# Kernel tuning notes

Hardware: AMD Instinct MI355X
Metric: run time of the kernel (lower is better)

## Reference

```python
import jax, jax.numpy as jnp
import numpy as np
from jax import lax

NUM_CLASSES = 102
IN_CAPS = 2592
IN_DIM = 8
OUT_DIM = 16
ROUTINGS = 3
IMG = 112

def squash(s, axis=-1, eps=1e-8):
    sq = jnp.sum(s * s, axis=axis, keepdims=True)
    return (sq / (1.0 + sq)) * s / jnp.sqrt(sq + eps)

def conv2d(x, w, b, stride):
    y = lax.conv_general_dilated(x, w, (stride, stride), 'VALID',
                                 dimension_numbers=('NCHW', 'OIHW', 'NCHW'))
    return y + b[None, :, None, None]

def setup_inputs() -> dict:
    key = jax.random.key(0)
    ks = jax.random.split(key, 12)
    B = 32
    x = jax.random.normal(ks[0], (B, 3, IMG, IMG), jnp.float32)
    targets = jax.random.randint(ks[1], (B,), 0, NUM_CLASSES)
    conv1_w = jax.random.normal(ks[2], (256, 3, 11, 11), jnp.float32) * 0.02
    conv1_b = jnp.zeros((256,), jnp.float32)
    pc_w = jax.random.normal(ks[3], (256, 256, 9, 9), jnp.float32) * 0.02
    pc_b = jnp.zeros((256,), jnp.float32)
    W = jax.random.normal(ks[4], (NUM_CLASSES, IN_CAPS, OUT_DIM, IN_DIM), jnp.float32) * 0.01
    fc1_w = jax.random.normal(ks[5], (NUM_CLASSES * OUT_DIM, 512), jnp.float32) * 0.02
    fc1_b = jnp.zeros((512,), jnp.float32)
    fc2_w = jax.random.normal(ks[6], (512, 1024), jnp.float32) * 0.02
    fc2_b = jnp.zeros((1024,), jnp.float32)
    fc3_w = jax.random.normal(ks[7], (1024, 3 * IMG * IMG), jnp.float32) * 0.02
    fc3_b = jnp.zeros((3 * IMG * IMG,), jnp.float32)
    return dict(x=x, targets=targets, conv1_w=conv1_w, conv1_b=conv1_b,
                pc_w=pc_w, pc_b=pc_b, W=W,
                fc1_w=fc1_w, fc1_b=fc1_b, fc2_w=fc2_w, fc2_b=fc2_b,
                fc3_w=fc3_w, fc3_b=fc3_b)

def reference(x, targets, conv1_w, conv1_b, pc_w, pc_b, W,
              fc1_w, fc1_b, fc2_w, fc2_b, fc3_w, fc3_b):
    B = x.shape[0]
    # conv backbone: [B,3,112,112] -> [B,256,34,34]
    feat = jax.nn.relu(conv2d(x, conv1_w, conv1_b, 3))
    # primary caps conv: -> [B,256,9,9] -> [B,2592,8], squash
    pc = conv2d(feat, pc_w, pc_b, 3)
    u = squash(pc.reshape(B, IN_CAPS, IN_DIM))
    # prediction vectors: [B, O, N, D_out]
    x_hat = jnp.einsum('ondi,bni->bond', W, u)
    x_hat_sg = lax.stop_gradient(x_hat)
    b = jnp.zeros((B, NUM_CLASSES, IN_CAPS), x.dtype)
    v = None
    for it in range(ROUTINGS):
        c = jax.nn.softmax(b, axis=1)  # couple over out caps
        xh = x_hat if it == ROUTINGS - 1 else x_hat_sg
        s = jnp.einsum('bon,bond->bod', c, xh)
        v = squash(s)
        if it < ROUTINGS - 1:
            b = b + jnp.einsum('bond,bod->bon', xh, v)
    # reconstruction: mask by target class capsule
    mask = jax.nn.one_hot(targets, NUM_CLASSES, dtype=v.dtype)
    h = (v * mask[:, :, None]).reshape(B, NUM_CLASSES * OUT_DIM)
    h = jax.nn.relu(h @ fc1_w + fc1_b)
    h = jax.nn.relu(h @ fc2_w + fc2_b)
    recon = jax.nn.sigmoid(h @ fc3_w + fc3_b).reshape(B, 3, IMG, IMG)
    return (v, recon)
```

## Files before the change

kernel.cpp:

```cpp
#include <hip/hip_runtime.h>
#include <hip/hip_fp16.h>
#include <math.h>

#define B32   32
#define OCLS  102
#define NCAPS 2592

#define OFF_FEAT   0u
#define OFF_C1WT   10027008u
#define OFF_PCWQ   10076160u
#define OFF_PCP    11780096u
#define OFF_WQ2    17088512u
#define OFF_WQ     25555456u
#define OFF_U2     34022400u
#define OFF_CT     34685952u
#define OFF_DEN    38916096u
#define OFF_S      38999040u
#define OFF_V0     39051264u
#define OFF_V1     39103488u
#define OFF_VSQ    39155712u
#define OFF_H1     39168768u
#define OFF_H2T    39185152u
#define OFF_FC3P   39217920u

typedef __attribute__((ext_vector_type(8))) short short8;
typedef __attribute__((ext_vector_type(4))) float f32x4;
typedef long long i64;

__device__ __forceinline__ unsigned short f2b(float f) {
  union { float f; unsigned u; } v; v.f = f;
  unsigned r = v.u + 0x7fffu + ((v.u >> 16) & 1u);
  return (unsigned short)(r >> 16);
}

__device__ __forceinline__ unsigned f2q_fast(float x) {
  union { float f; unsigned u; } v; v.f = x;
  unsigned s = (v.u >> 24) & 0x80u;
  unsigned au = v.u & 0x7fffffffu;
  if (au < 0x3c800000u) return s;
  if (au >= 0x43e00000u) return s | 0x7eu;
  unsigned r = au + 0x7ffffu + ((au >> 20) & 1u);
  unsigned e = (r >> 23) - 120u;
  unsigned m = (r >> 20) & 7u;
  return s | (e << 3) | m;
}

__device__ __forceinline__ unsigned fp8pair(float a, float b) {
#if __has_builtin(__builtin_amdgcn_cvt_pk_fp8_f32)
  return (unsigned)__builtin_amdgcn_cvt_pk_fp8_f32(a, b, 0, false) & 0xffffu;
#else
  return f2q_fast(a) | (f2q_fast(b) << 8);
#endif
}

__device__ __forceinline__ float rcpf(float x) {
#if __has_builtin(__builtin_amdgcn_rcpf)
  return __builtin_amdgcn_rcpf(x);
#else
  return 1.0f / x;
#endif
}

__global__ __launch_bounds__(256) void k_pack(const float* __restrict__ conv1_w,
                                              const float* __restrict__ pc_w,
                                              const float* __restrict__ W,
                                              unsigned short* __restrict__ C1WB,
                                              unsigned char* __restrict__ PCWQ,
                                              unsigned char* __restrict__ Wq2,
                                              unsigned char* __restrict__ Wq) {
  __shared__ unsigned char sq[32 * 128];
  int bb = blockIdx.x;
  int t = threadIdx.x;
  if (bb < 256) {
    if (t < 128) {
#pragma unroll
      for (int ci = 0; ci < 3; ++ci) {
        float v = (t < 121) ? conv1_w[bb * 363 + ci * 121 + t] : 0.f;
        C1WB[(ci * 256 + bb) * 128 + t] = f2b(v);
      }
    }
  } else if (bb < 512) {
    int co = bb - 256;
    for (int e = t; e < 20736; e += 256) {
      int ci = e / 81, tap = e - ci * 81;
      PCWQ[(size_t)ci * 26624 + co * 104 + tap] =
          (unsigned char)f2q_fast(pc_w[(size_t)co * 20736 + e] * 64.f);
    }
    for (int tap = 81; tap < 104; ++tap)
      PCWQ[(size_t)t * 26624 + co * 104 + tap] = 0;
  } else {
    size_t base = (size_t)(bb - 512) * 4096;
    const float4* src = (const float4*)(W + base + (size_t)t * 16);
    float4 f0 = src[0], f1 = src[1], f2 = src[2], f3 = src[3];
    float v[16] = {f0.x, f0.y, f0.z, f0.w, f1.x, f1.y, f1.z, f1.w,
                   f2.x, f2.y, f2.z, f2.w, f3.x, f3.y, f3.z, f3.w};
    unsigned words[4];
#pragma unroll
    for (int j = 0; j < 4; ++j)
      words[j] = fp8pair(v[4 * j] * 64.f, v[4 * j + 1] * 64.f) |
                 (fp8pair(v[4 * j + 2] * 64.f, v[4 * j + 3] * 64.f) << 16);
    *(uint4*)(Wq2 + base + (size_t)t * 16) =
        make_uint4(words[0], words[1], words[2], words[3]);
    int r = t >> 3, seg = t & 7;
#pragma unroll
    for (int e = 0; e < 16; ++e) {
      unsigned byte = (words[e >> 2] >> ((e & 3) * 8)) & 0xffu;
      int idx = seg * 16 + e, d = idx >> 3, i = idx & 7;
      sq[r * 128 + i * 16 + d] = (unsigned char)byte;
    }
    __syncthreads();
    *(uint4*)(Wq + base + (size_t)t * 16) = ((const uint4*)sq)[t];
  }
}

__global__ __launch_bounds__(256) void k_c1m(const float* __restrict__ x,
                                             const unsigned short* __restrict__ C1WB,
                                             const float* __restrict__ bias,
                                             float* __restrict__ feat2) {
  __shared__ unsigned short sh[48 * 128 + 128 * 128];
  unsigned short* lA = sh;
  unsigned short* lB = sh + 48 * 128;
  float* obuf = (float*)(sh + 48 * 128);

  int bx = blockIdx.x;
  int hf = blockIdx.y;
  int b = bx / 34, ho = bx % 34;
  int t = threadIdx.x;
  int lane = t & 63, wv = t >> 6;
  int l15 = lane & 15, lh = lane >> 4;
  int rx = l15 & 7;

  {
    uint4 zz = make_uint4(0, 0, 0, 0);
    uint4* z = (uint4*)lA;
    for (int i = t; i < 48 * 128 / 8; i += 256) z[i] = zz;
  }
  __syncthreads();

  f32x4 acc[3][2];
#pragma unroll
  for (int mf = 0; mf < 3; ++mf)
#pragma unroll
    for (int nf = 0; nf < 2; ++nf) acc[mf][nf] = (f32x4){0.f, 0.f, 0.f, 0.f};

#pragma unroll 1
  for (int ci = 0; ci < 3; ++ci) {
    {
      const uint4* Bsrc = (const uint4*)(C1WB + ci * 32768 + hf * 16384);
#pragma unroll
      for (int i = 0; i < 8; ++i) {
        int f = i * 256 + t;
        int row = f >> 4, cu = f & 15;
        ((uint4*)lB)[row * 16 + (cu ^ (row & 7))] = Bsrc[f];
      }
    }
    for (int tk = t; tk < 374; tk += 256) {
      int kh = tk / 34, wo = tk - kh * 34;
      const float* src = x + ((size_t)(b * 3 + ci) * 112 + ho * 3 + kh) * 112 + wo * 3;
#pragma unroll
      for (int j = 0; j < 11; ++j) {
        int tap = kh * 11 + j;
        int cu = tap >> 3;
        lA[wo * 128 + (((cu ^ (wo & 7)) << 3) | (tap & 7))] = f2b(src[j]);
      }
    }
    __syncthreads();

#pragma unroll
    for (int s = 0; s < 4; ++s) {
      int cub = ((s * 4 + lh) ^ rx) << 3;
      short8 a0 = *(const short8*)(lA + (0 + l15) * 128 + cub);
      short8 a1 = *(const short8*)(lA + (16 + l15) * 128 + cub);
      short8 a2 = *(const short8*)(lA + (32 + l15) * 128 + cub);
      short8 b0 = *(const short8*)(lB + (wv * 32 + 0 + l15) * 128 + cub);
      short8 b1 = *(const short8*)(lB + (wv * 32 + 16 + l15) * 128 + cub);
      acc[0][0] = __builtin_amdgcn_mfma_f32_16x16x32_bf16(a0, b0, acc[0][0], 0, 0, 0);
      acc[0][1] = __builtin_amdgcn_mfma_f32_16x16x32_bf16(a0, b1, acc[0][1], 0, 0, 0);
      acc[1][0] = __builtin_amdgcn_mfma_f32_16x16x32_bf16(a1, b0, acc[1][0], 0, 0, 0);
      acc[1][1] = __builtin_amdgcn_mfma_f32_16x16x32_bf16(a1, b1, acc[1][1], 0, 0, 0);
      acc[2][0] = __builtin_amdgcn_mfma_f32_16x16x32_bf16(a2, b0, acc[2][0], 0, 0, 0);
      acc[2][1] = __builtin_amdgcn_mfma_f32_16x16x32_bf16(a2, b1, acc[2][1], 0, 0, 0);
    }
    __syncthreads();
  }

  float bv[2];
#pragma unroll
  for (int nf = 0; nf < 2; ++nf) bv[nf] = bias[hf * 128 + wv * 32 + nf * 16 + l15];
#pragma unroll
  for (int mf = 0; mf < 3; ++mf)
#pragma unroll
    for (int nf = 0; nf < 2; ++nf)
#pragma unroll
      for (int r = 0; r < 4; ++r) {
        int wo = mf * 16 + lh * 4 + r;
        if (wo < 36)
          obuf[(wv * 32 + nf * 16 + l15) * 36 + wo] = fmaxf(acc[mf][nf][r] + bv[nf], 0.f);
      }
  __syncthreads();
  float4* dst = (float4*)(feat2 + (size_t)bx * 9216 + hf * 4608);
  const float4* srcb = (const float4*)obuf;
  for (int i = t; i < 1152; i += 256) dst[i] = srcb[i];
}

__device__ __forceinline__ void pc_gather8(const float* __restrict__ feat2,
                                           unsigned char* __restrict__ dstbuf,
                                           int mb, int ci, int t) {
  for (int task = t; task < 576; task += 256) {
    int m = task / 9, kh = task - m * 9;
    int gm = mb * 64 + m;
    if (gm < 2592) {
      int b = gm / 81, p = gm - b * 81;
      int ho = p / 9, wo = p - ho * 9;
      const float* src = feat2 + ((size_t)(b * 34 + ho * 3 + kh) * 256 + ci) * 36 + wo * 3;
      unsigned char* dst = dstbuf + m * 104 + kh * 9;
      unsigned p01 = fp8pair(src[0], src[1]);
      unsigned p23 = fp8pair(src[2], src[3]);
      unsigned p45 = fp8pair(src[4], src[5]);
      unsigned p67 = fp8pair(src[6], src[7]);
      unsigned p8  = fp8pair(src[8], 0.f);
      dst[0] = p01; dst[1] = p01 >> 8;
      dst[2] = p23; dst[3] = p23 >> 8;
      dst[4] = p45; dst[5] = p45 >> 8;
      dst[6] = p67; dst[7] = p67 >> 8;
      dst[8] = p8;
    }
  }
}

__global__ __launch_bounds__(256, 3) void k_pc4(const float* __restrict__ feat2,
                                                const unsigned char* __restrict__ PCWQ,
                                                __half* __restrict__ pcp) {
  __shared__ unsigned char lA[2][64 * 104];

  int mb = blockIdx.x, kc = blockIdx.y;
  int t = threadIdx.x;
  int lane = t & 63, wv = t >> 6;
  int l15 = lane & 15, lh = lane >> 4;

  {
    uint4 zz = make_uint4(0, 0, 0, 0);
    uint4* z = (uint4*)lA;
    for (int i = t; i < 2 * 64 * 104 / 16; i += 256) z[i] = zz;
  }
  __syncthreads();
  pc_gather8(feat2, lA[0], mb, kc * 16, t);
  __syncthreads();

  f32x4 acc[4][4];
#pragma unroll
  for (int mf = 0; mf < 4; ++mf)
#pragma unroll
    for (int nf = 0; nf < 4; ++nf) acc[mf][nf] = (f32x4){0.f, 0.f, 0.f, 0.f};

#pragma unroll 1
  for (int cil = 0; cil < 16; ++cil) {
    int ci = kc * 16 + cil;
    int cur = cil & 1;

    i64 bfr[4][3];
    const unsigned char* Bbase = PCWQ + (size_t)ci * 26624 + (wv * 64 + l15) * 104 + lh * 8;
#pragma unroll
    for (int nf = 0; nf < 4; ++nf)
#pragma unroll
      for (int s = 0; s < 3; ++s)
        bfr[nf][s] = *(const i64*)(Bbase + nf * 16 * 104 + s * 32);

    if (cil < 15) pc_gather8(feat2, lA[cur ^ 1], mb, ci + 1, t);

    const unsigned char* arow = lA[cur] + l15 * 104 + lh * 8;
#pragma unroll
    for (int s = 0; s < 3; ++s) {
      i64 a0 = *(const i64*)(arow + s * 32);
      i64 a1 = *(const i64*)(arow + 16 * 104 + s * 32);
      i64 a2 = *(const i64*)(arow + 32 * 104 + s * 32);
      i64 a3 = *(const i64*)(arow + 48 * 104 + s * 32);
      acc[0][0] = __builtin_amdgcn_mfma_f32_16x16x32_fp8_fp8(a0, bfr[0][s], acc[0][0], 0, 0, 0);
      acc[0][1] = __builtin_amdgcn_mfma_f32_16x16x32_fp8_fp8(a0, bfr[1][s], acc[0][1], 0, 0, 0);
      acc[0][2] = __builtin_amdgcn_mfma_f32_16x16x32_fp8_fp8(a0, bfr[2][s], acc[0][2], 0, 0, 0);
      acc[0][3] = __builtin_amdgcn_mfma_f32_16x16x32_fp8_fp8(a0, bfr[3][s], acc[0][3], 0, 0, 0);
      acc[1][0] = __builtin_amdgcn_mfma_f32_16x16x32_fp8_fp8(a1, bfr[0][s], acc[1][0], 0, 0, 0);
      acc[1][1] = __builtin_amdgcn_mfma_f32_16x16x32_fp8_fp8(a1, bfr[1][s], acc[1][1], 0, 0, 0);
      acc[1][2] = __builtin_amdgcn_mfma_f32_16x16x32_fp8_fp8(a1, bfr[2][s], acc[1][2], 0, 0, 0);
      acc[1][3] = __builtin_amdgcn_mfma_f32_16x16x32_fp8_fp8(a1, bfr[3][s], acc[1][3], 0, 0, 0);
      acc[2][0] = __builtin_amdgcn_mfma_f32_16x16x32_fp8_fp8(a2, bfr[0][s], acc[2][0], 0, 0, 0);
      acc[2][1] = __builtin_amdgcn_mfma_f32_16x16x32_fp8_fp8(a2, bfr[1][s], acc[2][1], 0, 0, 0);
      acc[2][2] = __builtin_amdgcn_mfma_f32_16x16x32_fp8_fp8(a2, bfr[2][s], acc[2][2], 0, 0, 0);
      acc[2][3] = __builtin_amdgcn_mfma_f32_16x16x32_fp8_fp8(a2, bfr[3][s], acc[2][3], 0, 0, 0);
      acc[3][0] = __builtin_amdgcn_mfma_f32_16x16x32_fp8_fp8(a3, bfr[0][s], acc[3][0], 0, 0, 0);
      acc[3][1] = __builtin_amdgcn_mfma_f32_16x16x32_fp8_fp8(a3, bfr[1][s], acc[3][1], 0, 0, 0);
      acc[3][2] = __builtin_amdgcn_mfma_f32_16x16x32_fp8_fp8(a3, bfr[2][s], acc[3][2], 0, 0, 0);
      acc[3][3] = __builtin_amdgcn_mfma_f32_16x16x32_fp8_fp8(a3, bfr[3][s], acc[3][3], 0, 0, 0);
    }
    __syncthreads();
  }

#pragma unroll
  for (int mf = 0; mf < 4; ++mf) {
    int gm = mb * 64 + mf * 16 + lh * 4;
    if (gm < 2592) {
      __half* dst = pcp + (size_t)kc * 663552 + (size_t)gm * 256 + wv * 64 + l15;
#pragma unroll
      for (int nf = 0; nf < 4; ++nf)
#pragma unroll
        for (int r = 0; r < 4; ++r)
          dst[(size_t)r * 256 + nf * 16] = __float2half(acc[mf][nf][r]);
    }
  }
}

__global__ __launch_bounds__(256) void k_rs(const __half* __restrict__ pcp,
                                            const float* __restrict__ pcb,
                                            float* __restrict__ u2) {
  __shared__ float tile[81 * 17];
  int b = blockIdx.x;
  int cog = blockIdx.y;
  int c0 = cog * 16;
  int t = threadIdx.x;

  for (int e = t; e < 1296; e += 256) {
    int p = e >> 4, col = e & 15;
    const __half* base = pcp + (size_t)(b * 81 + p) * 256 + c0 + col;
    float s = 0.f;
#pragma unroll
    for (int c = 0; c < 16; ++c) s += __half2float(base[(size_t)c * 663552]);
    tile[p * 17 + col] = pcb[c0 + col] + s * 0.015625f;
  }
  __syncthreads();

  if (t < 162) {
    float v[8];
    float sq = 0.f;
#pragma unroll
    for (int i = 0; i < 8; ++i) {
      int g = t * 8 + i;
      int col = g / 81, p = g - col * 81;
      v[i] = tile[p * 17 + col];
      sq += v[i] * v[i];
    }
    float sc = (sq / (1.f + sq)) / sqrtf(sq + 1e-8f);
    int n = cog * 162 + t;
    float4* dst = (float4*)(u2 + ((size_t)b * 2592 + n) * 8);
    dst[0] = make_float4(v[0] * sc, v[1] * sc, v[2] * sc, v[3] * sc);
    dst[1] = make_float4(v[4] * sc, v[5] * sc, v[6] * sc, v[7] * sc);
  }
}

__global__ __launch_bounds__(128) void k_A3(const unsigned char* __restrict__ Wq,
                                            const float* __restrict__ u2,
                                            const unsigned char* __restrict__ vq,
                                            __half* __restrict__ cT,
                                            float* __restrict__ den) {
  int nb = blockIdx.x;
  int ch = blockIdx.y;
  int o0 = ch * 34;
  int t = threadIdx.x, wv = t >> 6, lane = t & 63;
  int l15 = lane & 15, g = lane >> 4;
  int n0 = nb * 4 + 2 * wv;
  int nl = g >> 1, ih = (g & 1) * 4;

  float4 u0 = *(const float4*)(u2 + (((size_t)l15 * 2592 + n0 + nl) * 8 + ih));
  float4 u1 = *(const float4*)(u2 + (((size_t)(l15 + 16) * 2592 + n0 + nl) * 8 + ih));

  int nlA = l15 >> 3, iA = l15 & 7;
  const unsigned char* Ap = Wq + (((size_t)(n0 + nlA)) * 8 + iA) * 16 + (g & 1) * 8 +
                            (size_t)o0 * 331776;
  const unsigned char* B0p = vq + (size_t)l15 * 16 + (g & 1) * 8 + (size_t)o0 * 512;
  bool act = (g < 2);

  float den0 = 0.f, den1 = 0.f;
#pragma unroll 2
  for (int oo = 0; oo < 34; ++oo) {
    i64 a = 0, b0 = 0, b1 = 0;
    if (act) {
      a  = *(const i64*)(Ap + (size_t)oo * 331776);
      b0 = *(const i64*)(B0p + (size_t)oo * 512);
      b1 = *(const i64*)(B0p + (size_t)oo * 512 + 256);
    }
    f32x4 d0 = {0.f, 0.f, 0.f, 0.f}, d1 = {0.f, 0.f, 0.f, 0.f};
    d0 = __builtin_amdgcn_mfma_f32_16x16x32_fp8_fp8(a, b0, d0, 0, 0, 0);
    d1 = __builtin_amdgcn_mfma_f32_16x16x32_fp8_fp8(a, b1, d1, 0, 0, 0);
    float p0 = d0[0] * u0.x + d0[1] * u0.y + d0[2] * u0.z + d0[3] * u0.w;
    float p1 = d1[0] * u1.x + d1[1] * u1.y + d1[2] * u1.z + d1[3] * u1.w;
    p0 += __shfl_xor(p0, 16);
    p1 += __shfl_xor(p1, 16);
    p0 *= 1.52587890625e-05f;
    p1 *= 1.52587890625e-05f;
    float e0 = __expf(p0), e1 = __expf(p1);
    den0 += e0; den1 += e1;
    if ((g & 1) == 0) {
      __half* dst = cT + ((size_t)(o0 + oo) * 2592 + n0 + nl) * 32 + l15;
      dst[0]  = __float2half(e0);
      dst[16] = __float2half(e1);
    }
  }
  if ((g & 1) == 0) {
    atomicAdd(den + (n0 + nl) * 32 + l15, den0);
    atomicAdd(den + (n0 + nl) * 32 + l15 + 16, den1);
  }
}

__device__ __forceinline__ i64 cu_pack8(float c, float4 a, float4 b) {
  union { unsigned u[2]; i64 v; } r;
  r.u[0] = fp8pair(c * a.x, c * a.y) | (fp8pair(c * a.z, c * a.w) << 16);
  r.u[1] = fp8pair(c * b.x, c * b.y) | (fp8pair(c * b.z, c * b.w) << 16);
  return r.v;
}

template <bool HASC>
__global__ __launch_bounds__(256) void k_B3(const unsigned char* __restrict__ Wq2,
                                            const float* __restrict__ u2,
                                            const __half* __restrict__ cT,
                                            const float* __restrict__ den,
                                            float* __restrict__ s) {
  int o = blockIdx.x, kc = blockIdx.y;
  int t = threadIdx.x, lane = t & 63, wv = t >> 6;
  int l15 = lane & 15, h = lane >> 4;

  f32x4 acc0 = {0.f, 0.f, 0.f, 0.f}, acc1 = {0.f, 0.f, 0.f, 0.f};

#pragma unroll 1
  for (int st = wv; st < 54; st += 4) {
    int n = kc * 216 + st * 4 + h;
    i64 aq = *(const i64*)(Wq2 + (((size_t)o * 2592 + n) * 16 + l15) * 8);

    const float4* u0p = (const float4*)(u2 + ((size_t)l15 * 2592 + n) * 8);
    float4 u0a = u0p[0], u0b = u0p[1];
    const float4* u1p = (const float4*)(u2 + ((size_t)(l15 + 16) * 2592 + n) * 8);
    float4 u1a = u1p[0], u1b = u1p[1];

    float c0 = 16.0f, c1 = 16.0f;
    if (HASC) {
      const __half* cp = cT + ((size_t)o * 2592 + n) * 32;
      float i0 = rcpf(den[n * 32 + l15]);
      float i1 = rcpf(den[n * 32 + l15 + 16]);
      c0 = 16.0f * __half2float(cp[l15]) * i0;
      c1 = 16.0f * __half2float(cp[l15 + 16]) * i1;
    }
    i64 b0 = cu_pack8(c0, u0a, u0b);
    i64 b1 = cu_pack8(c1, u1a, u1b);

    acc0 = __builtin_amdgcn_mfma_f32_16x16x32_fp8_fp8(aq, b0, acc0, 0, 0, 0);
    acc1 = __builtin_amdgcn_mfma_f32_16x16x32_fp8_fp8(aq, b1, acc1, 0, 0, 0);
  }

#pragma unroll
  for (int r = 0; r < 4; ++r) {
    atomicAdd(s + ((size_t)l15 * 102 + o) * 16 + h * 4 + r, acc0[r]);
    atomicAdd(s + ((size_t)(l15 + 16) * 102 + o) * 16 + h * 4 + r, acc1[r]);
  }
}

__global__ void k_R(const float* __restrict__ s, float scale,
                    float* __restrict__ vout, const float* __restrict__ addin,
                    unsigned char* __restrict__ vsq, float* __restrict__ szero,
                    float* __restrict__ dzero) {
  int t = blockIdx.x * 256 + threadIdx.x;
  if (dzero) {
    for (int i = t; i < 82944; i += 3328) dzero[i] = 0.f;
  }
  if (t >= 3264) return;
  const float* sp = s + t * 16;
  float r[16];
  float sq = 0.f;
#pragma unroll
  for (int d = 0; d < 16; ++d) {
    r[d] = sp[d] * scale;
    sq += r[d] * r[d];
  }
  if (szero) {
#pragma unroll
    for (int d = 0; d < 16; ++d) szero[t * 16 + d] = 0.f;
  }
  float sc = (sq / (1.f + sq)) / sqrtf(sq + 1e-8f);
  float vv[16];
#pragma unroll
  for (int d = 0; d < 16; ++d) {
    vv[d] = r[d] * sc;
    vout[t * 16 + d] = vv[d];
  }
  if (vsq) {
    int b = t / 102, o = t - b * 102;
    float w[16];
#pragma unroll
    for (int d = 0; d < 16; ++d)
      w[d] = (addin ? (addin[t * 16 + d] + vv[d]) : vv[d]) * 1024.f;
    unsigned words[4];
#pragma unroll
    for (int q = 0; q < 4; ++q)
      words[q] = fp8pair(w[4 * q], w[4 * q + 1]) | (fp8pair(w[4 * q + 2], w[4 * q + 3]) << 16);
    *(uint4*)(vsq + ((size_t)o * 32 + b) * 16) =
        make_uint4(words[0], words[1], words[2], words[3]);
  }
}

__global__ void k_fc1(const float* __restrict__ v2, const int* __restrict__ tgt,
                      const float* __restrict__ w1, const float* __restrict__ b1,
                      float* __restrict__ h1) {
  int j = blockIdx.x * 128 + threadIdx.x;
  int bq = blockIdx.y;
#pragma unroll
  for (int bi = 0; bi < 4; ++bi) {
    int b = bq * 4 + bi;
    int tb = tgt[b];
    float acc = b1[j];
    const float* vv = v2 + (b * 102 + tb) * 16;
    const float* wr = w1 + (tb * 16) * 512 + j;
#pragma unroll
    for (int d = 0; d < 16; ++d) acc += vv[d] * wr[d * 512];
    h1[b * 512 + j] = fmaxf(acc, 0.f);
  }
}

__global__ void k_fc2(const float* __restrict__ h1, const float* __restrict__ w2,
                      const float* __restrict__ b2, float* __restrict__ h2T) {
  int j = blockIdx.x * 128 + threadIdx.x;
  int bq = blockIdx.y;
  float acc[4];
#pragma unroll
  for (int bi = 0; bi < 4; ++bi) acc[bi] = b2[j];
  for (int k = 0; k < 512; ++k) {
    float wv = w2[k * 1024 + j];
#pragma unroll
    for (int bi = 0; bi < 4; ++bi) acc[bi] += h1[(bq * 4 + bi) * 512 + k] * wv;
  }
  float4 o;
  o.x = fmaxf(acc[0], 0.f); o.y = fmaxf(acc[1], 0.f);
  o.z = fmaxf(acc[2], 0.f); o.w = fmaxf(acc[3], 0.f);
  *(float4*)(h2T + j * 32 + bq * 4) = o;
}

__global__ void k_fc3a(const float* __restrict__ h2T, const float* __restrict__ w3,
                       float* __restrict__ p) {
  int j = blockIdx.x * 128 + threadIdx.x;
  int ky = blockIdx.y;
  float acc[32];
#pragma unroll
  for (int i = 0; i < 32; ++i) acc[i] = 0.f;
  int k0 = ky * 256;
  for (int k = k0; k < k0 + 256; ++k) {
    float wv = w3[(size_t)k * 37632 + j];
    const float4* hp = (const float4*)(h2T + k * 32);
#pragma unroll
    for (int q = 0; q < 8; ++q) {
      float4 h = hp[q];
      acc[q * 4 + 0] += h.x * wv; acc[q * 4 + 1] += h.y * wv;
      acc[q * 4 + 2] += h.z * wv; acc[q * 4 + 3] += h.w * wv;
    }
  }
#pragma unroll
  for (int i = 0; i < 32; ++i)
    p[((size_t)ky * 32 + i) * 37632 + j] = acc[i];
}

__global__ void k_fc3b(const float* __restrict__ p, const float* __restrict__ b3,
                       float* __restrict__ out) {
  int j = blockIdx.x * 256 + threadIdx.x;
  float bv = b3[j];
#pragma unroll 1
  for (int b = 0; b < 32; ++b) {
    float s = bv + p[(size_t)b * 37632 + j] + p[(size_t)(32 + b) * 37632 + j] +
              p[(size_t)(64 + b) * 37632 + j] + p[(size_t)(96 + b) * 37632 + j];
    out[52224 + (size_t)b * 37632 + j] = 1.0f / (1.0f + __expf(-s));
  }
}

extern "C" void kernel_launch(void* const* d_in, const int* in_sizes, int n_in,
                              void* d_out, int out_size, void* d_ws, size_t ws_size,
                              hipStream_t stream) {
  const float* x       = (const float*)d_in[0];
  const int*   targets = (const int*)d_in[1];
  const float* conv1_w = (const float*)d_in[2];
  const float* conv1_b = (const float*)d_in[3];
  const float* pc_w    = (const float*)d_in[4];
  const float* pc_b    = (const float*)d_in[5];
  const float* W       = (const float*)d_in[6];
  const float* fc1_w   = (const float*)d_in[7];
  const float* fc1_b   = (const float*)d_in[8];
  const float* fc2_w   = (const float*)d_in[9];
  const float* fc2_b   = (const float*)d_in[10];
  const float* fc3_w   = (const float*)d_in[11];
  const float* fc3_b   = (const float*)d_in[12];
  float* out = (float*)d_out;
  float* ws = (float*)d_ws;

  float* FEAT2 = ws + OFF_FEAT;
  unsigned short* C1WB = (unsigned short*)(ws + OFF_C1WT);
  unsigned char* PCWQ = (unsigned char*)(ws + OFF_PCWQ);
  __half* PCP = (__half*)(ws + OFF_PCP);
  unsigned char* WQ2 = (unsigned char*)(ws + OFF_WQ2);
  unsigned char* WQ  = (unsigned char*)(ws + OFF_WQ);
  float* U2   = ws + OFF_U2;
  __half* CT  = (__half*)(ws + OFF_CT);
  float* DEN  = ws + OFF_DEN;
  float* S    = ws + OFF_S;
  float* V0   = ws + OFF_V0;
  float* V1   = ws + OFF_V1;
  unsigned char* VSQ = (unsigned char*)(ws + OFF_VSQ);
  float* H1   = ws + OFF_H1;
  float* H2T  = ws + OFF_H2T;
  float* FC3P = ws + OFF_FC3P;

  k_pack<<<dim3(8774), 256, 0, stream>>>(conv1_w, pc_w, W, C1WB, PCWQ, WQ2, WQ);

  k_c1m<<<dim3(1088, 2), 256, 0, stream>>>(x, C1WB, conv1_b, FEAT2);

  k_pc4<<<dim3(41, 16), 256, 0, stream>>>(FEAT2, PCWQ, PCP);
  k_rs<<<dim3(32, 16), 256, 0, stream>>>(PCP, pc_b, U2);

  hipMemsetAsync(S, 0, 52224 * sizeof(float), stream);
  k_B3<false><<<dim3(102, 12), 256, 0, stream>>>(WQ2, U2, nullptr, nullptr, S);
  k_R<<<dim3(13), 256, 0, stream>>>(S, 1.0f / (102.0f * 1024.0f), V0, nullptr, VSQ, S, DEN);

  k_A3<<<dim3(648, 3), 128, 0, stream>>>(WQ, U2, VSQ, CT, DEN);
  k_B3<true><<<dim3(102, 12), 256, 0, stream>>>(WQ2, U2, CT, DEN, S);
  k_R<<<dim3(13), 256, 0, stream>>>(S, 1.0f / 1024.0f, V1, V0, VSQ, S, DEN);

  k_A3<<<dim3(648, 3), 128, 0, stream>>>(WQ, U2, VSQ, CT, DEN);
  k_B3<true><<<dim3(102, 12), 256, 0, stream>>>(WQ2, U2, CT, DEN, S);
  k_R<<<dim3(13), 256, 0, stream>>>(S, 1.0f / 1024.0f, out, nullptr, nullptr, nullptr, nullptr);

  k_fc1<<<dim3(4, 8), 128, 0, stream>>>(out, targets, fc1_w, fc1_b, H1);
  k_fc2<<<dim3(8, 8), 128, 0, stream>>>(H1, fc2_w, fc2_b, H2T);
  k_fc3a<<<dim3(294, 4), 128, 0, stream>>>(H2T, fc3_w, FC3P);
  k_fc3b<<<dim3(147), 256, 0, stream>>>(FC3P, fc3_b, out);
}
```

Before: 549.4 us.

## Fuse fc1/fc2, fold S memset into pack, and double per-block W packing

Merges the fc1 and fc2 kernels into one kernel that keeps h1 in shared memory, which removes a launch and a global round-trip. The hipMemsetAsync of S becomes extra blocks in k_pack. Each k_pack block now converts two rows of W, halving the block count. The fused fc kernel runs on only 8 blocks of 512 threads, so the fc2 stage may lose parallelism compared with the earlier 64 blocks.

```diff
diff --git a/kernel.cpp b/kernel.cpp
--- a/kernel.cpp
+++ b/kernel.cpp
@@ -19,7 +19,6 @@
 #define OFF_V0     39051264u
 #define OFF_V1     39103488u
 #define OFF_VSQ    39155712u
-#define OFF_H1     39168768u
 #define OFF_H2T    39185152u
 #define OFF_FC3P   39217920u
 
@@ -67,8 +66,9 @@
                                               unsigned short* __restrict__ C1WB,
                                               unsigned char* __restrict__ PCWQ,
                                               unsigned char* __restrict__ Wq2,
-                                              unsigned char* __restrict__ Wq) {
-  __shared__ unsigned char sq[32 * 128];
+                                              unsigned char* __restrict__ Wq,
+                                              float* __restrict__ S) {
+  __shared__ unsigned char sq[64 * 128];
   int bb = blockIdx.x;
   int t = threadIdx.x;
   if (bb < 256) {
@@ -88,28 +88,39 @@
     }
     for (int tap = 81; tap < 104; ++tap)
       PCWQ[(size_t)t * 26624 + co * 104 + tap] = 0;
-  } else {
-    size_t base = (size_t)(bb - 512) * 4096;
-    const float4* src = (const float4*)(W + base + (size_t)t * 16);
-    float4 f0 = src[0], f1 = src[1], f2 = src[2], f3 = src[3];
-    float v[16] = {f0.x, f0.y, f0.z, f0.w, f1.x, f1.y, f1.z, f1.w,
-                   f2.x, f2.y, f2.z, f2.w, f3.x, f3.y, f3.z, f3.w};
-    unsigned words[4];
-#pragma unroll
-    for (int j = 0; j < 4; ++j)
-      words[j] = fp8pair(v[4 * j] * 64.f, v[4 * j + 1] * 64.f) |
-                 (fp8pair(v[4 * j + 2] * 64.f, v[4 * j + 3] * 64.f) << 16);
-    *(uint4*)(Wq2 + base + (size_t)t * 16) =
-        make_uint4(words[0], words[1], words[2], words[3]);
-    int r = t >> 3, seg = t & 7;
+  } else if (bb < 4643) {
+    size_t base = (size_t)(bb - 512) * 8192;
+    int g = t >> 3, seg = t & 7;
+    int r0 = 2 * g, r1 = 2 * g + 1;
+    const f32x4* s0 = (const f32x4*)(W + base + r0 * 128 + seg * 16);
+    const f32x4* s1 = (const f32x4*)(W + base + r1 * 128 + seg * 16);
+    f32x4 a0 = s0[0], a1 = s0[1], a2 = s0[2], a3 = s0[3];
+    f32x4 c0 = s1[0], c1 = s1[1], c2 = s1[2], c3 = s1[3];
+    asm volatile("" :: "v"(a0), "v"(a1), "v"(a2), "v"(a3),
+                       "v"(c0), "v"(c1), "v"(c2), "v"(c3));
+    unsigned w0[4], w1[4];
+    f32x4 va[4] = {a0, a1, a2, a3}, vc[4] = {c0, c1, c2, c3};
+#pragma unroll
+    for (int j = 0; j < 4; ++j) {
+      w0[j] = fp8pair(va[j][0] * 64.f, va[j][1] * 64.f) |
+              (fp8pair(va[j][2] * 64.f, va[j][3] * 64.f) << 16);
+      w1[j] = fp8pair(vc[j][0] * 64.f, vc[j][1] * 64.f) |
+              (fp8pair(vc[j][2] * 64.f, vc[j][3] * 64.f) << 16);
+    }
+    *(uint4*)(Wq2 + base + r0 * 128 + seg * 16) = make_uint4(w0[0], w0[1], w0[2], w0[3]);
+    *(uint4*)(Wq2 + base + r1 * 128 + seg * 16) = make_uint4(w1[0], w1[1], w1[2], w1[3]);
 #pragma unroll
     for (int e = 0; e < 16; ++e) {
-      unsigned byte = (words[e >> 2] >> ((e & 3) * 8)) & 0xffu;
       int idx = seg * 16 + e, d = idx >> 3, i = idx & 7;
-      sq[r * 128 + i * 16 + d] = (unsigned char)byte;
+      sq[r0 * 128 + i * 16 + d] = (unsigned char)((w0[e >> 2] >> ((e & 3) * 8)) & 0xffu);
+      sq[r1 * 128 + i * 16 + d] = (unsigned char)((w1[e >> 2] >> ((e & 3) * 8)) & 0xffu);
     }
     __syncthreads();
     *(uint4*)(Wq + base + (size_t)t * 16) = ((const uint4*)sq)[t];
+    *(uint4*)(Wq + base + 4096 + (size_t)t * 16) = ((const uint4*)sq)[256 + t];
+  } else {
+    int idx = (bb - 4643) * 1024 + t * 4;
+    *(float4*)(S + idx) = make_float4(0.f, 0.f, 0.f, 0.f);
   }
 }
 
@@ -494,40 +505,47 @@
   }
 }
 
-__global__ void k_fc1(const float* __restrict__ v2, const int* __restrict__ tgt,
-                      const float* __restrict__ w1, const float* __restrict__ b1,
-                      float* __restrict__ h1) {
-  int j = blockIdx.x * 128 + threadIdx.x;
-  int bq = blockIdx.y;
+__global__ __launch_bounds__(512) void k_fc12(const float* __restrict__ v2,
+                                              const int* __restrict__ tgt,
+                                              const float* __restrict__ w1,
+                                              const float* __restrict__ b1,
+                                              const float* __restrict__ w2,
+                                              const float* __restrict__ b2,
+                                              float* __restrict__ h2T) {
+  __shared__ float h1s[4][512];
+  int bq = blockIdx.x;
+  int t = threadIdx.x;
 #pragma unroll
   for (int bi = 0; bi < 4; ++bi) {
     int b = bq * 4 + bi;
     int tb = tgt[b];
-    float acc = b1[j];
+    float acc = b1[t];
     const float* vv = v2 + (b * 102 + tb) * 16;
-    const float* wr = w1 + (tb * 16) * 512 + j;
+    const float* wr = w1 + (tb * 16) * 512 + t;
 #pragma unroll
     for (int d = 0; d < 16; ++d) acc += vv[d] * wr[d * 512];
-    h1[b * 512 + j] = fmaxf(acc, 0.f);
-  }
-}
-
-__global__ void k_fc2(const float* __restrict__ h1, const float* __restrict__ w2,
-                      const float* __restrict__ b2, float* __restrict__ h2T) {
-  int j = blockIdx.x * 128 + threadIdx.x;
-  int bq = blockIdx.y;
-  float acc[4];
-#pragma unroll
-  for (int bi = 0; bi < 4; ++bi) acc[bi] = b2[j];
+    h1s[bi][t] = fmaxf(acc, 0.f);
+  }
+  __syncthreads();
+  float a0[4], a1[4];
+#pragma unroll
+  for (int bi = 0; bi < 4; ++bi) { a0[bi] = b2[t]; a1[bi] = b2[t + 512]; }
   for (int k = 0; k < 512; ++k) {
-    float wv = w2[k * 1024 + j];
-#pragma unroll
-    for (int bi = 0; bi < 4; ++bi) acc[bi] += h1[(bq * 4 + bi) * 512 + k] * wv;
-  }
-  float4 o;
-  o.x = fmaxf(acc[0], 0.f); o.y = fmaxf(acc[1], 0.f);
-  o.z = fmaxf(acc[2], 0.f); o.w = fmaxf(acc[3], 0.f);
-  *(float4*)(h2T + j * 32 + bq * 4) = o;
+    float w0 = w2[k * 1024 + t], w1v = w2[k * 1024 + t + 512];
+#pragma unroll
+    for (int bi = 0; bi < 4; ++bi) {
+      float h = h1s[bi][k];
+      a0[bi] += h * w0;
+      a1[bi] += h * w1v;
+    }
+  }
+  float4 o0, o1;
+  o0.x = fmaxf(a0[0], 0.f); o0.y = fmaxf(a0[1], 0.f);
+  o0.z = fmaxf(a0[2], 0.f); o0.w = fmaxf(a0[3], 0.f);
+  o1.x = fmaxf(a1[0], 0.f); o1.y = fmaxf(a1[1], 0.f);
+  o1.z = fmaxf(a1[2], 0.f); o1.w = fmaxf(a1[3], 0.f);
+  *(float4*)(h2T + t * 32 + bq * 4) = o0;
+  *(float4*)(h2T + (t + 512) * 32 + bq * 4) = o1;
 }
 
 __global__ void k_fc3a(const float* __restrict__ h2T, const float* __restrict__ w3,
@@ -597,18 +615,16 @@
   float* V0   = ws + OFF_V0;
   float* V1   = ws + OFF_V1;
   unsigned char* VSQ = (unsigned char*)(ws + OFF_VSQ);
-  float* H1   = ws + OFF_H1;
   float* H2T  = ws + OFF_H2T;
   float* FC3P = ws + OFF_FC3P;
 
-  k_pack<<<dim3(8774), 256, 0, stream>>>(conv1_w, pc_w, W, C1WB, PCWQ, WQ2, WQ);
+  k_pack<<<dim3(4694), 256, 0, stream>>>(conv1_w, pc_w, W, C1WB, PCWQ, WQ2, WQ, S);
 
   k_c1m<<<dim3(1088, 2), 256, 0, stream>>>(x, C1WB, conv1_b, FEAT2);
 
   k_pc4<<<dim3(41, 16), 256, 0, stream>>>(FEAT2, PCWQ, PCP);
   k_rs<<<dim3(32, 16), 256, 0, stream>>>(PCP, pc_b, U2);
 
-  hipMemsetAsync(S, 0, 52224 * sizeof(float), stream);
   k_B3<false><<<dim3(102, 12), 256, 0, stream>>>(WQ2, U2, nullptr, nullptr, S);
   k_R<<<dim3(13), 256, 0, stream>>>(S, 1.0f / (102.0f * 1024.0f), V0, nullptr, VSQ, S, DEN);
 
@@ -620,8 +636,7 @@
   k_B3<true><<<dim3(102, 12), 256, 0, stream>>>(WQ2, U2, CT, DEN, S);
   k_R<<<dim3(13), 256, 0, stream>>>(S, 1.0f / 1024.0f, out, nullptr, nullptr, nullptr, nullptr);
 
-  k_fc1<<<dim3(4, 8), 128, 0, stream>>>(out, targets, fc1_w, fc1_b, H1);
-  k_fc2<<<dim3(8, 8), 128, 0, stream>>>(H1, fc2_w, fc2_b, H2T);
+  k_fc12<<<dim3(8), 512, 0, stream>>>(out, targets, fc1_w, fc1_b, fc2_w, fc2_b, H2T);
   k_fc3a<<<dim3(294, 4), 128, 0, stream>>>(H2T, fc3_w, FC3P);
   k_fc3b<<<dim3(147), 256, 0, stream>>>(FC3P, fc3_b, out);
 }
```

Measured after the change: 545.4 us. About the same (-0.7%).
